# Performance work log

Hardware: AMD Instinct MI355X
Metric: run time of the kernel (lower is better)

The kernel has to match this reference:

```python
import jax, jax.numpy as jnp
import numpy as np

NUM_ENTS = 100000
NUM_RELS2 = 1000  # num_rels * 2
H_DIM = 128
NUM_EDGES = 2000000
RRELU_SLOPE = (1.0 / 8.0 + 1.0 / 3.0) / 2.0  # F.rrelu eval-mode negative slope


def l2_normalize(x, eps=1e-12):
    # F.normalize along last dim
    n = jnp.sqrt(jnp.sum(x * x, axis=-1, keepdims=True))
    return x / jnp.maximum(n, eps)


def setup_inputs() -> dict:
    key = jax.random.key(0)
    ks = jax.random.split(key, 11)
    s = 1.0 / np.sqrt(H_DIM)
    return {
        "ent_emb": jax.random.normal(ks[0], (NUM_ENTS, H_DIM), jnp.float32),
        "rel_emb": jax.random.normal(ks[1], (NUM_RELS2, H_DIM), jnp.float32) * s,
        "his": jax.random.normal(ks[2], (NUM_ENTS, H_DIM), jnp.float32),
        "W_neighbor": jax.random.normal(ks[3], (H_DIM, H_DIM), jnp.float32) * s,
        "W_self": jax.random.normal(ks[4], (H_DIM, H_DIM), jnp.float32) * s,
        "time_gate_weight": jax.random.normal(ks[5], (H_DIM, H_DIM), jnp.float32) * s,
        "time_gate_bias": jnp.zeros((H_DIM,), jnp.float32),
        "edge_norm": jax.random.uniform(ks[6], (NUM_EDGES,), jnp.float32),
        "src": jax.random.randint(ks[7], (NUM_EDGES,), 0, NUM_ENTS, jnp.int32),
        "dst": jax.random.randint(ks[8], (NUM_EDGES,), 0, NUM_ENTS, jnp.int32),
        "etype": jax.random.randint(ks[9], (NUM_EDGES,), 0, NUM_RELS2, jnp.int32),
    }


def reference(ent_emb, rel_emb, his, W_neighbor, W_self, time_gate_weight,
              time_gate_bias, edge_norm, src, dst, etype):
    # layer_norm=True branch: L2-normalize entity embeddings (F.normalize)
    h = l2_normalize(ent_emb)                                   # [N, D]
    # UnionRGCNLayer message: (h[src] + rel_emb[etype]) @ W, scaled by edge norm
    node = h[src] + rel_emb[etype]                              # [E, D] gather
    msg = (node @ W_neighbor) * edge_norm[:, None]              # [E, D]
    agg = jax.ops.segment_sum(msg, dst, num_segments=NUM_ENTS)  # [N, D] scatter
    # self-loop + rrelu (eval mode: leaky with mean slope)
    h_cur = agg + h @ W_self
    h_cur = jnp.where(h_cur >= 0, h_cur, RRELU_SLOPE * h_cur)
    # time gate: blend current with historical embedding
    gate = jax.nn.sigmoid(h_cur @ time_gate_weight + time_gate_bias)
    out = gate * h_cur + (1.0 - gate) * his
    return out
```

## Files before the change

kernel.cpp:

```cpp
#include <hip/hip_runtime.h>
#include <math.h>

#define NUM_ENTS   100000
#define HD         128
#define NUM_EDGES  2000000
#define NUM_RELS2  1000
#define RRELU_SLOPE 0.22916666666666666f
#define NBLK 391
#define NPAD (NBLK * 256)
#define EQ4  (NUM_EDGES / 4)
#define EBLK ((EQ4 + 255) / 256)

#define SB_CNT 391
#define SB_HB  25000
#define SB_RB  125
#define SB_WP  24
#define SB_TOTAL (SB_CNT + SB_HB + SB_RB + SB_WP)

typedef __attribute__((ext_vector_type(8))) short bf16x8;
typedef __attribute__((ext_vector_type(4))) float f32x4;

__device__ __forceinline__ float bf2f(unsigned short h) {
    union { unsigned int u; float f; } v;
    v.u = ((unsigned int)h) << 16;
    return v.f;
}
__device__ __forceinline__ void unpack2(unsigned int u, float& lo, float& hi) {
    union { unsigned int u; float f; } a, b;
    a.u = u << 16;
    b.u = u & 0xffff0000u;
    lo = a.f; hi = b.f;
}
__device__ __forceinline__ unsigned short f2bf(float f) {
    union { float f; unsigned int u; } v; v.f = f;
    unsigned int r = 0x7fffu + ((v.u >> 16) & 1u);
    return (unsigned short)((v.u + r) >> 16);
}

__global__ void __launch_bounds__(256)
setup_kernel(const float* __restrict__ ent, const float* __restrict__ rel,
             const float* __restrict__ Wn, const float* __restrict__ Ws,
             const float* __restrict__ Wt,
             int* __restrict__ cnt, unsigned short* __restrict__ hb,
             unsigned short* __restrict__ rb, unsigned short* __restrict__ Wp) {
    const int bid = blockIdx.x, tid = threadIdx.x;
    if (bid < SB_CNT) {
        cnt[bid * 256 + tid] = 0;
    } else if (bid < SB_CNT + SB_HB) {
        const int row = (bid - SB_CNT) * 4 + (tid >> 6);
        const int lane = tid & 63;
        const float2 v = *(const float2*)(ent + (size_t)row * HD + lane * 2);
        float ss = v.x * v.x + v.y * v.y;
        #pragma unroll
        for (int m = 1; m < 64; m <<= 1) ss += __shfl_xor(ss, m, 64);
        const float inv = 1.0f / fmaxf(sqrtf(ss), 1e-12f);
        const unsigned int o = (unsigned int)f2bf(v.x * inv) |
                               ((unsigned int)f2bf(v.y * inv) << 16);
        *(unsigned int*)(hb + (size_t)row * HD + lane * 2) = o;
    } else if (bid < SB_CNT + SB_HB + SB_RB) {
        const int i = (bid - SB_CNT - SB_HB) * 256 + tid;
        const float4 v = ((const float4*)rel)[i];
        ushort4 o;
        o.x = f2bf(v.x); o.y = f2bf(v.y); o.z = f2bf(v.z); o.w = f2bf(v.w);
        ((ushort4*)rb)[i] = o;
    } else {
        const int blk = (bid - SB_CNT - SB_HB - SB_RB) * 4 + (tid >> 6);
        const int lane = tid & 63;
        const int w = blk >> 5, rem = blk & 31, t = rem >> 2, kt = rem & 3;
        const float* W = (w == 0) ? Wn : (w == 1) ? Ws : Wt;
        const int n  = t * 16 + (lane & 15);
        const int k0 = kt * 32 + (lane >> 4) * 8;
        unsigned short tmp[8];
        #pragma unroll
        for (int j = 0; j < 8; ++j) tmp[j] = f2bf(W[(size_t)(k0 + j) * HD + n]);
        unsigned short* d = Wp + ((size_t)blk * 64 + lane) * 8;
        *(ushort4*)(d + 0) = make_ushort4(tmp[0], tmp[1], tmp[2], tmp[3]);
        *(ushort4*)(d + 4) = make_ushort4(tmp[4], tmp[5], tmp[6], tmp[7]);
    }
}

__global__ void __launch_bounds__(256)
hist_kernel(const int* __restrict__ dst, int* __restrict__ cnt, int* __restrict__ pos) {
    const int i = blockIdx.x * 256 + threadIdx.x;
    if (i < EQ4) {
        const int4 d4 = ((const int4*)dst)[i];
        int4 p4;
        p4.x = atomicAdd(&cnt[d4.x], 1);
        p4.y = atomicAdd(&cnt[d4.y], 1);
        p4.z = atomicAdd(&cnt[d4.z], 1);
        p4.w = atomicAdd(&cnt[d4.w], 1);
        ((int4*)pos)[i] = p4;
    }
}

__global__ void __launch_bounds__(256)
scan1_kernel(const int* __restrict__ cnt, int* __restrict__ offs, int* __restrict__ bsum) {
    __shared__ int tmp[256];
    const int t = threadIdx.x;
    const int i = blockIdx.x * 256 + t;
    const int v = cnt[i];
    tmp[t] = v;
    __syncthreads();
    #pragma unroll
    for (int d = 1; d < 256; d <<= 1) {
        const int a = (t >= d) ? tmp[t - d] : 0;
        __syncthreads();
        tmp[t] += a;
        __syncthreads();
    }
    offs[i] = tmp[t] - v;
    if (t == 255) bsum[blockIdx.x] = tmp[255];
}

__global__ void __launch_bounds__(512)
scan2_kernel(int* __restrict__ bsum) {
    __shared__ int tmp[512];
    const int t = threadIdx.x;
    const int v = (t < NBLK) ? bsum[t] : 0;
    tmp[t] = v;
    __syncthreads();
    #pragma unroll
    for (int d = 1; d < 512; d <<= 1) {
        const int a = (t >= d) ? tmp[t - d] : 0;
        __syncthreads();
        tmp[t] += a;
        __syncthreads();
    }
    if (t < NBLK) bsum[t] = tmp[t] - v;
}

__global__ void __launch_bounds__(256)
scan3_kernel(int* __restrict__ offs, const int* __restrict__ bsum) {
    const int i = blockIdx.x * 256 + threadIdx.x;
    offs[i] += bsum[blockIdx.x];
}

__global__ void __launch_bounds__(256)
permute_kernel(const int* __restrict__ dst, const int* __restrict__ src,
               const int* __restrict__ ety, const float* __restrict__ enorm,
               const int* __restrict__ offs, const int* __restrict__ pos,
               uint2* __restrict__ recs) {
    const int i = blockIdx.x * 256 + threadIdx.x;
    if (i < EQ4) {
        const int4 d4 = ((const int4*)dst)[i];
        const int4 s4 = ((const int4*)src)[i];
        const int4 t4 = ((const int4*)ety)[i];
        const float4 n4 = ((const float4*)enorm)[i];
        const int4 p4 = ((const int4*)pos)[i];
        recs[offs[d4.x] + p4.x] = make_uint2((unsigned int)s4.x | ((unsigned int)t4.x << 17), __float_as_uint(n4.x));
        recs[offs[d4.y] + p4.y] = make_uint2((unsigned int)s4.y | ((unsigned int)t4.y << 17), __float_as_uint(n4.y));
        recs[offs[d4.z] + p4.z] = make_uint2((unsigned int)s4.z | ((unsigned int)t4.z << 17), __float_as_uint(n4.z));
        recs[offs[d4.w] + p4.w] = make_uint2((unsigned int)s4.w | ((unsigned int)t4.w << 17), __float_as_uint(n4.w));
    }
}

__device__ __forceinline__ void accum8(float* acc, uint4 hv, uint4 rv, float w) {
    float h0, h1, r0, r1;
    unpack2(hv.x, h0, h1); unpack2(rv.x, r0, r1);
    acc[0] += (h0 + r0) * w; acc[1] += (h1 + r1) * w;
    unpack2(hv.y, h0, h1); unpack2(rv.y, r0, r1);
    acc[2] += (h0 + r0) * w; acc[3] += (h1 + r1) * w;
    unpack2(hv.z, h0, h1); unpack2(rv.z, r0, r1);
    acc[4] += (h0 + r0) * w; acc[5] += (h1 + r1) * w;
    unpack2(hv.w, h0, h1); unpack2(rv.w, r0, r1);
    acc[6] += (h0 + r0) * w; acc[7] += (h1 + r1) * w;
}

__global__ void __launch_bounds__(256, 4)
gather_mfma(const unsigned short* __restrict__ hb,
            const unsigned short* __restrict__ rb,
            const int* __restrict__ offs,
            const uint2* __restrict__ recs,
            const unsigned short* __restrict__ Wp,
            const float* __restrict__ bias,
            const float* __restrict__ his,
            float* __restrict__ out) {
    __shared__ unsigned short T[16 * 136];
    const int tid = threadIdx.x;
    const int m0 = blockIdx.x * 16;
    const int grp = tid >> 4, sub = tid & 15;
    const int wv = tid >> 6, lane = tid & 63;
    const int rA = lane & 15, quad = lane >> 4;
    const unsigned short* hbp = hb + sub * 8;
    const unsigned short* rbp = rb + sub * 8;

    {
        const int d = m0 + grp;
        const int beg = offs[d], end = offs[d + 1];
        float acc[8] = {0.f, 0.f, 0.f, 0.f, 0.f, 0.f, 0.f, 0.f};
        int i = beg;
        uint2 rcA[4];
        #pragma unroll
        for (int k = 0; k < 4; ++k) rcA[k] = recs[min(i + k, NUM_EDGES - 1)];
        while (__any(i < end)) {
            uint2 rcB[4];
            #pragma unroll
            for (int k = 0; k < 4; ++k) rcB[k] = recs[min(i + 4 + k, NUM_EDGES - 1)];
            uint4 hv[4], rv[4]; float w[4];
            #pragma unroll
            for (int k = 0; k < 4; ++k) {
                w[k] = (i + k) < end ? __uint_as_float(rcA[k].y) : 0.f;
                hv[k] = *(const uint4*)(hbp + (size_t)(rcA[k].x & 0x1FFFFu) * HD);
                rv[k] = *(const uint4*)(rbp + (size_t)(rcA[k].x >> 17) * HD);
            }
            #pragma unroll
            for (int k = 0; k < 4; ++k) accum8(acc, hv[k], rv[k], w[k]);
            #pragma unroll
            for (int k = 0; k < 4; ++k) rcA[k] = rcB[k];
            i += 4;
        }
        unsigned short* dT = T + grp * 136 + sub * 8;
        *(ushort4*)(dT + 0) = make_ushort4(f2bf(acc[0]), f2bf(acc[1]), f2bf(acc[2]), f2bf(acc[3]));
        *(ushort4*)(dT + 4) = make_ushort4(f2bf(acc[4]), f2bf(acc[5]), f2bf(acc[6]), f2bf(acc[7]));
    }
    __syncthreads();

    const bf16x8* WF = (const bf16x8*)Wp;
    bf16x8 a1[4], a2[4];
    #pragma unroll
    for (int kt = 0; kt < 4; ++kt)
        a1[kt] = *(const bf16x8*)(T + rA * 136 + kt * 32 + quad * 8);
    {
        const unsigned short* base = hb + (size_t)(m0 + rA) * HD + quad * 8;
        #pragma unroll
        for (int kt = 0; kt < 4; ++kt)
            a2[kt] = *(const bf16x8*)(base + kt * 32);
    }

    f32x4 acc1[2];
    #pragma unroll
    for (int tt = 0; tt < 2; ++tt) acc1[tt] = (f32x4)0.f;

    #pragma unroll
    for (int tt = 0; tt < 2; ++tt) {
        const int t = wv * 2 + tt;
        #pragma unroll
        for (int kt = 0; kt < 4; ++kt) {
            const bf16x8 bfr = WF[(size_t)(t * 4 + kt) * 64 + lane];
            acc1[tt] = __builtin_amdgcn_mfma_f32_16x16x32_bf16(a1[kt], bfr, acc1[tt], 0, 0, 0);
        }
        #pragma unroll
        for (int kt = 0; kt < 4; ++kt) {
            const bf16x8 bfr = WF[(size_t)(32 + t * 4 + kt) * 64 + lane];
            acc1[tt] = __builtin_amdgcn_mfma_f32_16x16x32_bf16(a2[kt], bfr, acc1[tt], 0, 0, 0);
        }
    }

    #pragma unroll
    for (int tt = 0; tt < 2; ++tt)
        #pragma unroll
        for (int r = 0; r < 4; ++r)
            acc1[tt][r] = acc1[tt][r] >= 0.f ? acc1[tt][r] : RRELU_SLOPE * acc1[tt][r];

    __syncthreads();
    #pragma unroll
    for (int tt = 0; tt < 2; ++tt)
        #pragma unroll
        for (int r = 0; r < 4; ++r)
            T[(quad * 4 + r) * 136 + (wv * 2 + tt) * 16 + rA] = f2bf(acc1[tt][r]);
    __syncthreads();

    bf16x8 a3[4];
    #pragma unroll
    for (int kt = 0; kt < 4; ++kt)
        a3[kt] = *(const bf16x8*)(T + rA * 136 + kt * 32 + quad * 8);

    #pragma unroll
    for (int tt = 0; tt < 2; ++tt) {
        const int t = wv * 2 + tt;
        const float bn = bias[t * 16 + rA];
        f32x4 c2 = (f32x4){bn, bn, bn, bn};
        #pragma unroll
        for (int kt = 0; kt < 4; ++kt) {
            const bf16x8 bfr = WF[(size_t)(64 + t * 4 + kt) * 64 + lane];
            c2 = __builtin_amdgcn_mfma_f32_16x16x32_bf16(a3[kt], bfr, c2, 0, 0, 0);
        }
        const int col = t * 16 + rA;
        #pragma unroll
        for (int r = 0; r < 4; ++r) {
            const size_t row = (size_t)(m0 + quad * 4 + r);
            const float g = 1.f / (1.f + __expf(-c2[r]));
            const float h = his[row * HD + col];
            out[row * HD + col] = g * acc1[tt][r] + (1.f - g) * h;
        }
    }
}

extern "C" void kernel_launch(void* const* d_in, const int* in_sizes, int n_in,
                              void* d_out, int out_size, void* d_ws, size_t ws_size,
                              hipStream_t stream) {
    const float* ent   = (const float*)d_in[0];
    const float* rel   = (const float*)d_in[1];
    const float* his   = (const float*)d_in[2];
    const float* Wn    = (const float*)d_in[3];
    const float* Ws    = (const float*)d_in[4];
    const float* Wt    = (const float*)d_in[5];
    const float* bias  = (const float*)d_in[6];
    const float* enorm = (const float*)d_in[7];
    const int* src = (const int*)d_in[8];
    const int* dst = (const int*)d_in[9];
    const int* ety = (const int*)d_in[10];
    float* out = (float*)d_out;

    char* p = (char*)d_ws;
    unsigned short* hb = (unsigned short*)p;  p += (size_t)NUM_ENTS * HD * 2;
    unsigned short* rb = (unsigned short*)p;  p += (size_t)NUM_RELS2 * HD * 2;
    unsigned short* Wp = (unsigned short*)p;  p += (size_t)96 * 64 * 8 * 2;
    int* cnt  = (int*)p;                      p += (size_t)NPAD * 4;
    int* offs = (int*)p;                      p += (size_t)NPAD * 4;
    int* bsum = (int*)p;                      p += 512 * 4;
    int* pos  = (int*)p;                      p += (size_t)NUM_EDGES * 4;
    uint2* recs = (uint2*)p;

    setup_kernel<<<SB_TOTAL, 256, 0, stream>>>(ent, rel, Wn, Ws, Wt, cnt, hb, rb, Wp);
    hist_kernel<<<EBLK, 256, 0, stream>>>(dst, cnt, pos);
    scan1_kernel<<<NBLK, 256, 0, stream>>>(cnt, offs, bsum);
    scan2_kernel<<<1, 512, 0, stream>>>(bsum);
    scan3_kernel<<<NBLK, 256, 0, stream>>>(offs, bsum);
    permute_kernel<<<EBLK, 256, 0, stream>>>(dst, src, ety, enorm, offs, pos, recs);
    gather_mfma<<<NUM_ENTS / 16, 256, 0, stream>>>(hb, rb, offs, recs, Wp, bias, his, out);
}
```

Baseline: 423.2 us.

## Fuse histogram into setup kernel, memset counts, and per-thread gather loop exit

The dst histogram atomics now run inside the setup kernel alongside the normalize and convert blocks, so one launch is removed and the two phases overlap. The count array is now cleared with hipMemsetAsync, which has to finish before setup runs. The permute kernel processes two int4 groups per thread at half the grid size. The gather loop now exits per thread instead of waiting on a wave-wide __any, which lets lanes with fewer edges drop out early but may add divergence.

```diff
diff --git a/kernel.cpp b/kernel.cpp
--- a/kernel.cpp
+++ b/kernel.cpp
@@ -10,12 +10,13 @@
 #define NPAD (NBLK * 256)
 #define EQ4  (NUM_EDGES / 4)
 #define EBLK ((EQ4 + 255) / 256)
-
-#define SB_CNT 391
-#define SB_HB  25000
-#define SB_RB  125
-#define SB_WP  24
-#define SB_TOTAL (SB_CNT + SB_HB + SB_RB + SB_WP)
+#define PBLK ((EQ4 + 511) / 512)
+
+#define SB_HIST EBLK
+#define SB_HB   25000
+#define SB_RB   125
+#define SB_WP   24
+#define SB_TOTAL (SB_HIST + SB_HB + SB_RB + SB_WP)
 
 typedef __attribute__((ext_vector_type(8))) short bf16x8;
 typedef __attribute__((ext_vector_type(4))) float f32x4;
@@ -40,14 +41,24 @@
 __global__ void __launch_bounds__(256)
 setup_kernel(const float* __restrict__ ent, const float* __restrict__ rel,
              const float* __restrict__ Wn, const float* __restrict__ Ws,
-             const float* __restrict__ Wt,
-             int* __restrict__ cnt, unsigned short* __restrict__ hb,
+             const float* __restrict__ Wt, const int* __restrict__ dst,
+             int* __restrict__ cnt, int* __restrict__ pos,
+             unsigned short* __restrict__ hb,
              unsigned short* __restrict__ rb, unsigned short* __restrict__ Wp) {
     const int bid = blockIdx.x, tid = threadIdx.x;
-    if (bid < SB_CNT) {
-        cnt[bid * 256 + tid] = 0;
-    } else if (bid < SB_CNT + SB_HB) {
-        const int row = (bid - SB_CNT) * 4 + (tid >> 6);
+    if (bid < SB_HIST) {
+        const int i = bid * 256 + tid;
+        if (i < EQ4) {
+            const int4 d4 = ((const int4*)dst)[i];
+            int4 p4;
+            p4.x = atomicAdd(&cnt[d4.x], 1);
+            p4.y = atomicAdd(&cnt[d4.y], 1);
+            p4.z = atomicAdd(&cnt[d4.z], 1);
+            p4.w = atomicAdd(&cnt[d4.w], 1);
+            ((int4*)pos)[i] = p4;
+        }
+    } else if (bid < SB_HIST + SB_HB) {
+        const int row = (bid - SB_HIST) * 4 + (tid >> 6);
         const int lane = tid & 63;
         const float2 v = *(const float2*)(ent + (size_t)row * HD + lane * 2);
         float ss = v.x * v.x + v.y * v.y;
@@ -57,14 +68,14 @@
         const unsigned int o = (unsigned int)f2bf(v.x * inv) |
                                ((unsigned int)f2bf(v.y * inv) << 16);
         *(unsigned int*)(hb + (size_t)row * HD + lane * 2) = o;
-    } else if (bid < SB_CNT + SB_HB + SB_RB) {
-        const int i = (bid - SB_CNT - SB_HB) * 256 + tid;
+    } else if (bid < SB_HIST + SB_HB + SB_RB) {
+        const int i = (bid - SB_HIST - SB_HB) * 256 + tid;
         const float4 v = ((const float4*)rel)[i];
         ushort4 o;
         o.x = f2bf(v.x); o.y = f2bf(v.y); o.z = f2bf(v.z); o.w = f2bf(v.w);
         ((ushort4*)rb)[i] = o;
     } else {
-        const int blk = (bid - SB_CNT - SB_HB - SB_RB) * 4 + (tid >> 6);
+        const int blk = (bid - SB_HIST - SB_HB - SB_RB) * 4 + (tid >> 6);
         const int lane = tid & 63;
         const int w = blk >> 5, rem = blk & 31, t = rem >> 2, kt = rem & 3;
         const float* W = (w == 0) ? Wn : (w == 1) ? Ws : Wt;
@@ -76,20 +87,6 @@
         unsigned short* d = Wp + ((size_t)blk * 64 + lane) * 8;
         *(ushort4*)(d + 0) = make_ushort4(tmp[0], tmp[1], tmp[2], tmp[3]);
         *(ushort4*)(d + 4) = make_ushort4(tmp[4], tmp[5], tmp[6], tmp[7]);
-    }
-}
-
-__global__ void __launch_bounds__(256)
-hist_kernel(const int* __restrict__ dst, int* __restrict__ cnt, int* __restrict__ pos) {
-    const int i = blockIdx.x * 256 + threadIdx.x;
-    if (i < EQ4) {
-        const int4 d4 = ((const int4*)dst)[i];
-        int4 p4;
-        p4.x = atomicAdd(&cnt[d4.x], 1);
-        p4.y = atomicAdd(&cnt[d4.y], 1);
-        p4.z = atomicAdd(&cnt[d4.z], 1);
-        p4.w = atomicAdd(&cnt[d4.w], 1);
-        ((int4*)pos)[i] = p4;
     }
 }
 
@@ -140,17 +137,20 @@
                const int* __restrict__ ety, const float* __restrict__ enorm,
                const int* __restrict__ offs, const int* __restrict__ pos,
                uint2* __restrict__ recs) {
-    const int i = blockIdx.x * 256 + threadIdx.x;
-    if (i < EQ4) {
-        const int4 d4 = ((const int4*)dst)[i];
-        const int4 s4 = ((const int4*)src)[i];
-        const int4 t4 = ((const int4*)ety)[i];
-        const float4 n4 = ((const float4*)enorm)[i];
-        const int4 p4 = ((const int4*)pos)[i];
-        recs[offs[d4.x] + p4.x] = make_uint2((unsigned int)s4.x | ((unsigned int)t4.x << 17), __float_as_uint(n4.x));
-        recs[offs[d4.y] + p4.y] = make_uint2((unsigned int)s4.y | ((unsigned int)t4.y << 17), __float_as_uint(n4.y));
-        recs[offs[d4.z] + p4.z] = make_uint2((unsigned int)s4.z | ((unsigned int)t4.z << 17), __float_as_uint(n4.z));
-        recs[offs[d4.w] + p4.w] = make_uint2((unsigned int)s4.w | ((unsigned int)t4.w << 17), __float_as_uint(n4.w));
+    #pragma unroll
+    for (int u = 0; u < 2; ++u) {
+        const int i = blockIdx.x * 512 + u * 256 + threadIdx.x;
+        if (i < EQ4) {
+            const int4 d4 = ((const int4*)dst)[i];
+            const int4 s4 = ((const int4*)src)[i];
+            const int4 t4 = ((const int4*)ety)[i];
+            const float4 n4 = ((const float4*)enorm)[i];
+            const int4 p4 = ((const int4*)pos)[i];
+            recs[offs[d4.x] + p4.x] = make_uint2((unsigned int)s4.x | ((unsigned int)t4.x << 17), __float_as_uint(n4.x));
+            recs[offs[d4.y] + p4.y] = make_uint2((unsigned int)s4.y | ((unsigned int)t4.y << 17), __float_as_uint(n4.y));
+            recs[offs[d4.z] + p4.z] = make_uint2((unsigned int)s4.z | ((unsigned int)t4.z << 17), __float_as_uint(n4.z));
+            recs[offs[d4.w] + p4.w] = make_uint2((unsigned int)s4.w | ((unsigned int)t4.w << 17), __float_as_uint(n4.w));
+        }
     }
 }
 
@@ -189,25 +189,26 @@
         const int beg = offs[d], end = offs[d + 1];
         float acc[8] = {0.f, 0.f, 0.f, 0.f, 0.f, 0.f, 0.f, 0.f};
         int i = beg;
-        uint2 rcA[4];
-        #pragma unroll
-        for (int k = 0; k < 4; ++k) rcA[k] = recs[min(i + k, NUM_EDGES - 1)];
-        while (__any(i < end)) {
-            uint2 rcB[4];
+        if (i < end) {
+            uint2 rcA[4];
             #pragma unroll
-            for (int k = 0; k < 4; ++k) rcB[k] = recs[min(i + 4 + k, NUM_EDGES - 1)];
-            uint4 hv[4], rv[4]; float w[4];
-            #pragma unroll
-            for (int k = 0; k < 4; ++k) {
-                w[k] = (i + k) < end ? __uint_as_float(rcA[k].y) : 0.f;
-                hv[k] = *(const uint4*)(hbp + (size_t)(rcA[k].x & 0x1FFFFu) * HD);
-                rv[k] = *(const uint4*)(rbp + (size_t)(rcA[k].x >> 17) * HD);
+            for (int k = 0; k < 4; ++k) rcA[k] = recs[min(i + k, NUM_EDGES - 1)];
+            for (; i < end; i += 4) {
+                uint2 rcB[4];
+                #pragma unroll
+                for (int k = 0; k < 4; ++k) rcB[k] = recs[min(i + 4 + k, NUM_EDGES - 1)];
+                uint4 hv[4], rv[4]; float w[4];
+                #pragma unroll
+                for (int k = 0; k < 4; ++k) {
+                    w[k] = (i + k) < end ? __uint_as_float(rcA[k].y) : 0.f;
+                    hv[k] = *(const uint4*)(hbp + (size_t)(rcA[k].x & 0x1FFFFu) * HD);
+                    rv[k] = *(const uint4*)(rbp + (size_t)(rcA[k].x >> 17) * HD);
+                }
+                #pragma unroll
+                for (int k = 0; k < 4; ++k) accum8(acc, hv[k], rv[k], w[k]);
+                #pragma unroll
+                for (int k = 0; k < 4; ++k) rcA[k] = rcB[k];
             }
-            #pragma unroll
-            for (int k = 0; k < 4; ++k) accum8(acc, hv[k], rv[k], w[k]);
-            #pragma unroll
-            for (int k = 0; k < 4; ++k) rcA[k] = rcB[k];
-            i += 4;
         }
         unsigned short* dT = T + grp * 136 + sub * 8;
         *(ushort4*)(dT + 0) = make_ushort4(f2bf(acc[0]), f2bf(acc[1]), f2bf(acc[2]), f2bf(acc[3]));
@@ -312,11 +313,11 @@
     int* pos  = (int*)p;                      p += (size_t)NUM_EDGES * 4;
     uint2* recs = (uint2*)p;
 
-    setup_kernel<<<SB_TOTAL, 256, 0, stream>>>(ent, rel, Wn, Ws, Wt, cnt, hb, rb, Wp);
-    hist_kernel<<<EBLK, 256, 0, stream>>>(dst, cnt, pos);
+    hipMemsetAsync(cnt, 0, (size_t)NPAD * 4, stream);
+    setup_kernel<<<SB_TOTAL, 256, 0, stream>>>(ent, rel, Wn, Ws, Wt, dst, cnt, pos, hb, rb, Wp);
     scan1_kernel<<<NBLK, 256, 0, stream>>>(cnt, offs, bsum);
     scan2_kernel<<<1, 512, 0, stream>>>(bsum);
     scan3_kernel<<<NBLK, 256, 0, stream>>>(offs, bsum);
-    permute_kernel<<<EBLK, 256, 0, stream>>>(dst, src, ety, enorm, offs, pos, recs);
+    permute_kernel<<<PBLK, 256, 0, stream>>>(dst, src, ety, enorm, offs, pos, recs);
     gather_mfma<<<NUM_ENTS / 16, 256, 0, stream>>>(hb, rb, offs, recs, Wp, bias, his, out);
 }
```

Result: faster. 411.4 us (-2.8%).
